# Performance work log

Measured on AMD Instinct MI355X. Metric: run time of the kernel, lower is better.

The kernel has to match this reference:

```python
import jax, jax.numpy as jnp
import numpy as np

N_PP, BATCH, BITS = 54, 16384, 108  # 54 partial products of a 54x54 array multiplier, 108-bit lanes


def setup_inputs() -> dict:
    key = jax.random.key(0)
    # bits are {0,1} floats, LSB-first along the last axis
    pps = jax.random.randint(key, (N_PP, BATCH, BITS), 0, 2).astype(jnp.float32)
    return {"pps": pps}


def _ripple_add(a, b):
    """Bit-exact ripple-carry add over last (bits) axis, LSB first.

    a, b: [..., BITS] with values in {0,1}. Returns (sum [..., BITS], carry_out [...]).
    Boolean full adder expressed arithmetically so it is differentiable:
      xor(x,y) = x + y - 2xy ; and(x,y) = xy ; or(x,y) = x + y - xy
    """
    aT = jnp.moveaxis(a, -1, 0)  # [BITS, ...]
    bT = jnp.moveaxis(b, -1, 0)
    c0 = jnp.zeros(a.shape[:-1], a.dtype)

    def full_adder(c, ab):
        ai, bi = ab
        axb = ai + bi - 2.0 * ai * bi          # a XOR b
        s = axb + c - 2.0 * axb * c            # (a XOR b) XOR c
        g = ai * bi                            # generate
        p = axb * c                            # propagate AND carry
        c_next = g + p - g * p                 # g OR p
        return c_next, s

    c_out, sT = jax.lax.scan(full_adder, c0, (aT, bT))
    return jnp.moveaxis(sT, 0, -1), c_out


def reference(pps):
    """Sequential (mode='sequential') accumulation of partial products.

    pps: [N_PP, ..., BITS]. result = (((pp0 + pp1) + pp2) + ...), bit-exact,
    carry-out dropped at each step exactly as in the torch module.
    """
    def step(res, p):
        s, _ = _ripple_add(res, p)
        return s, None

    out, _ = jax.lax.scan(step, pps[0], pps[1:])
    return out
```

## Files before the change

### kernel.cpp

```cpp
#include <hip/hip_runtime.h>


#define N_PP    54
#define BITS    108
#define BATCH   16384
#define TB      32
#define THREADS 256
#define ROW_F4  (BITS / 4)
#define CHUNK_F4 (TB * ROW_F4)
#define SLOTS   4

__global__ __launch_bounds__(THREADS)
void ppacc_kernel(const float* __restrict__ pps, float* __restrict__ out) {
    __shared__ float counts[TB][BITS + 1];

    const int tid = threadIdx.x;
    const int b0  = blockIdx.x * TB;

    float4 acc[SLOTS];
#pragma unroll
    for (int s = 0; s < SLOTS; ++s) acc[s] = make_float4(0.f, 0.f, 0.f, 0.f);

    const float4* base = reinterpret_cast<const float4*>(pps) + (size_t)b0 * ROW_F4;
    const size_t  pstride = (size_t)BATCH * ROW_F4;

    for (int p = 0; p < N_PP; ++p) {
        const float4* plane = base + (size_t)p * pstride;
#pragma unroll
        for (int s = 0; s < SLOTS; ++s) {
            const int idx = tid + s * THREADS;
            if (idx < CHUNK_F4) {
                float4 v = plane[idx];
                acc[s].x += v.x;
                acc[s].y += v.y;
                acc[s].z += v.z;
                acc[s].w += v.w;
            }
        }
    }

#pragma unroll
    for (int s = 0; s < SLOTS; ++s) {
        const int idx = tid + s * THREADS;
        if (idx < CHUNK_F4) {
            const int b   = idx / ROW_F4;
            const int bit = (idx % ROW_F4) * 4;
            counts[b][bit + 0] = acc[s].x;
            counts[b][bit + 1] = acc[s].y;
            counts[b][bit + 2] = acc[s].z;
            counts[b][bit + 3] = acc[s].w;
        }
    }
    __syncthreads();

    if (tid < TB) {
        int c = 0;
#pragma unroll
        for (int i = 0; i < BITS; ++i) {
            const int t = (int)counts[tid][i] + c;
            counts[tid][i] = (float)(t & 1);
            c = t >> 1;
        }
    }
    __syncthreads();

    float4* outp = reinterpret_cast<float4*>(out) + (size_t)b0 * ROW_F4;
#pragma unroll
    for (int s = 0; s < SLOTS; ++s) {
        const int idx = tid + s * THREADS;
        if (idx < CHUNK_F4) {
            const int b   = idx / ROW_F4;
            const int bit = (idx % ROW_F4) * 4;
            float4 v;
            v.x = counts[b][bit + 0];
            v.y = counts[b][bit + 1];
            v.z = counts[b][bit + 2];
            v.w = counts[b][bit + 3];
            outp[idx] = v;
        }
    }
}

extern "C" void kernel_launch(void* const* d_in, const int* in_sizes, int n_in,
                              void* d_out, int out_size, void* d_ws, size_t ws_size,
                              hipStream_t stream) {
    const float* pps = (const float*)d_in[0];
    float* out = (float*)d_out;
    const int grid = BATCH / TB;
    ppacc_kernel<<<grid, THREADS, 0, stream>>>(pps, out);
}
```

Measured before the change: 517.4 us.

## Split column counting and carry propagation into two kernels with prefetched loads

The fused kernel is replaced by two kernels. The first sums the 54 planes per float4 element over the flat plane, with software-prefetched loads and two elements per thread. The second resolves carries per batch row in registers, one thread per row, writing the result in place. This drops the shared-memory staging and the serial 32-thread carry phase that left most of each block idle. In exchange it adds a second launch and a full write and read of the count buffer through global memory.

```diff
diff --git a/kernel.cpp b/kernel.cpp
--- a/kernel.cpp
+++ b/kernel.cpp
@@ -1,91 +1,69 @@
 #include <hip/hip_runtime.h>
 
 
-#define N_PP    54
-#define BITS    108
-#define BATCH   16384
-#define TB      32
-#define THREADS 256
-#define ROW_F4  (BITS / 4)
-#define CHUNK_F4 (TB * ROW_F4)
-#define SLOTS   4
+#define N_PP   54
+#define BITS   108
+#define BATCH  16384
+#define ROW_F4 (BITS / 4)
+#define PLANE_F4 ((size_t)BATCH * ROW_F4)
 
-__global__ __launch_bounds__(THREADS)
-void ppacc_kernel(const float* __restrict__ pps, float* __restrict__ out) {
-    __shared__ float counts[TB][BITS + 1];
+__global__ __launch_bounds__(256)
+void count_kernel(const float4* __restrict__ pps, float4* __restrict__ cnt) {
+    const size_t i0 = (size_t)blockIdx.x * 512 + threadIdx.x;
+    const size_t i1 = i0 + 256;
 
-    const int tid = threadIdx.x;
-    const int b0  = blockIdx.x * TB;
+    float4 a0 = make_float4(0.f, 0.f, 0.f, 0.f);
+    float4 a1 = a0;
 
-    float4 acc[SLOTS];
+    const float4* p = pps;
+    float4 v0 = p[i0];
+    float4 v1 = p[i1];
+    for (int q = 1; q < N_PP; ++q) {
+        p += PLANE_F4;
+        float4 n0 = p[i0];
+        float4 n1 = p[i1];
+        a0.x += v0.x; a0.y += v0.y; a0.z += v0.z; a0.w += v0.w;
+        a1.x += v1.x; a1.y += v1.y; a1.z += v1.z; a1.w += v1.w;
+        v0 = n0; v1 = n1;
+    }
+    a0.x += v0.x; a0.y += v0.y; a0.z += v0.z; a0.w += v0.w;
+    a1.x += v1.x; a1.y += v1.y; a1.z += v1.z; a1.w += v1.w;
+
+    cnt[i0] = a0;
+    cnt[i1] = a1;
+}
+
+__global__ __launch_bounds__(64)
+void carry_kernel(float4* __restrict__ buf) {
+    const int row = blockIdx.x * 64 + threadIdx.x;
+    float4* rp = buf + (size_t)row * ROW_F4;
+
+    float r[BITS];
 #pragma unroll
-    for (int s = 0; s < SLOTS; ++s) acc[s] = make_float4(0.f, 0.f, 0.f, 0.f);
+    for (int j = 0; j < ROW_F4; ++j) {
+        reinterpret_cast<float4*>(r)[j] = rp[j];
+    }
 
-    const float4* base = reinterpret_cast<const float4*>(pps) + (size_t)b0 * ROW_F4;
-    const size_t  pstride = (size_t)BATCH * ROW_F4;
-
-    for (int p = 0; p < N_PP; ++p) {
-        const float4* plane = base + (size_t)p * pstride;
+    int c = 0;
 #pragma unroll
-        for (int s = 0; s < SLOTS; ++s) {
-            const int idx = tid + s * THREADS;
-            if (idx < CHUNK_F4) {
-                float4 v = plane[idx];
-                acc[s].x += v.x;
-                acc[s].y += v.y;
-                acc[s].z += v.z;
-                acc[s].w += v.w;
-            }
-        }
+    for (int i = 0; i < BITS; ++i) {
+        const int t = (int)r[i] + c;
+        r[i] = (float)(t & 1);
+        c = t >> 1;
     }
 
 #pragma unroll
-    for (int s = 0; s < SLOTS; ++s) {
-        const int idx = tid + s * THREADS;
-        if (idx < CHUNK_F4) {
-            const int b   = idx / ROW_F4;
-            const int bit = (idx % ROW_F4) * 4;
-            counts[b][bit + 0] = acc[s].x;
-            counts[b][bit + 1] = acc[s].y;
-            counts[b][bit + 2] = acc[s].z;
-            counts[b][bit + 3] = acc[s].w;
-        }
-    }
-    __syncthreads();
-
-    if (tid < TB) {
-        int c = 0;
-#pragma unroll
-        for (int i = 0; i < BITS; ++i) {
-            const int t = (int)counts[tid][i] + c;
-            counts[tid][i] = (float)(t & 1);
-            c = t >> 1;
-        }
-    }
-    __syncthreads();
-
-    float4* outp = reinterpret_cast<float4*>(out) + (size_t)b0 * ROW_F4;
-#pragma unroll
-    for (int s = 0; s < SLOTS; ++s) {
-        const int idx = tid + s * THREADS;
-        if (idx < CHUNK_F4) {
-            const int b   = idx / ROW_F4;
-            const int bit = (idx % ROW_F4) * 4;
-            float4 v;
-            v.x = counts[b][bit + 0];
-            v.y = counts[b][bit + 1];
-            v.z = counts[b][bit + 2];
-            v.w = counts[b][bit + 3];
-            outp[idx] = v;
-        }
+    for (int j = 0; j < ROW_F4; ++j) {
+        rp[j] = reinterpret_cast<float4*>(r)[j];
     }
 }
 
 extern "C" void kernel_launch(void* const* d_in, const int* in_sizes, int n_in,
                               void* d_out, int out_size, void* d_ws, size_t ws_size,
                               hipStream_t stream) {
-    const float* pps = (const float*)d_in[0];
-    float* out = (float*)d_out;
-    const int grid = BATCH / TB;
-    ppacc_kernel<<<grid, THREADS, 0, stream>>>(pps, out);
+    const float4* pps = (const float4*)d_in[0];
+    float4* out = (float4*)d_out;
+
+    count_kernel<<<(int)(PLANE_F4 / 512), 256, 0, stream>>>(pps, out);
+    carry_kernel<<<BATCH / 64, 64, 0, stream>>>(out);
 }
```

New measurement: 502.9 us. -2.8%, faster.
